# Kernel optimization log

Measured on AMD Instinct MI355X. Metric: run time of the kernel, lower is better.

Reference implementation:

```python
import jax, jax.numpy as jnp
import numpy as np

N_NODES = 100000
N_EDGES = 1600000
FEAT = 64
HID = 64
N_LAYERS = 3
N_GRAPHS = 500


def setup_inputs() -> dict:
    key = jax.random.key(0)
    ks = jax.random.split(key, 8)
    x = jax.random.normal(ks[0], (N_NODES, FEAT), dtype=jnp.float32)
    edge_index = jax.random.randint(ks[1], (2, N_EDGES), 0, N_NODES, dtype=jnp.int64)
    mask = jax.random.randint(ks[2], (N_NODES,), 0, 2).astype(bool)
    batch = jnp.sort(jax.random.randint(ks[3], (N_NODES,), 0, N_GRAPHS, dtype=jnp.int64))
    Ws = jax.random.normal(ks[4], (N_LAYERS, HID, HID), dtype=jnp.float32) * 0.1
    bs = jnp.zeros((N_LAYERS, HID), dtype=jnp.float32)
    lt1_w = jax.random.normal(ks[5], (HID, 1), dtype=jnp.float32) * 0.1
    lt1_b = jnp.zeros((1,), dtype=jnp.float32)
    return {"x": x, "edge_index": edge_index, "mask": mask, "batch": batch,
            "Ws": Ws, "bs": bs, "lt1_w": lt1_w, "lt1_b": lt1_b}


def reference(x, edge_index, mask, batch, Ws, bs, lt1_w, lt1_b):
    n = x.shape[0]
    self_loop = jnp.arange(n, dtype=edge_index.dtype)
    src = jnp.concatenate([edge_index[0], self_loop])  # [E+N]
    dst = jnp.concatenate([edge_index[1], self_loop])
    # GCN symmetric normalization with self loops
    deg = jax.ops.segment_sum(jnp.ones_like(dst, dtype=x.dtype), dst, num_segments=n)
    dis = jax.lax.rsqrt(deg)  # deg >= 1 thanks to self loops
    norm = (dis[src] * dis[dst])[:, None]  # [E+N, 1]

    h = x
    for i in range(N_LAYERS):
        h = h @ Ws[i]                                   # [N, H] linear (no bias)
        msg = h[src] * norm                              # gather + scale
        h = jax.ops.segment_sum(msg, dst, num_segments=n) + bs[i]  # scatter-add + bias
        h = jax.nn.elu(h)
        # F.dropout with training=False is identity (eval mode)

    # global_mean_pool over masked nodes per graph
    m = mask.astype(h.dtype)
    num = jax.ops.segment_sum(h * m[:, None], batch, num_segments=N_GRAPHS)
    den = jax.ops.segment_sum(m, batch, num_segments=N_GRAPHS)
    pooled = num / jnp.maximum(den, 1.0)[:, None]        # [G, H]
    return pooled @ lt1_w + lt1_b                        # [G, 1]
```

## Files before the change

kernel.cpp:

```cpp
#include <hip/hip_runtime.h>
#include <math.h>

#define N_NODES 100000
#define N_EDGES 1600000
#define HID 64
#define N_LAYERS 3
#define N_GRAPHS 500

#define BUK_SHIFT 9
#define BUK_NODES 512
#define NBUK ((N_NODES + BUK_NODES - 1) / BUK_NODES)
#define BIN_BLOCKS 256
#define CHUNK ((N_EDGES + BIN_BLOCKS - 1) / BIN_BLOCKS)
#define PSRC_CAP (N_EDGES + 8 * N_NODES)

#define TM 64
#define LDX 68

typedef _Float16 half_t;
union H4 { ushort4 u; half_t h[4]; };

__device__ __forceinline__ float elu_f(float x) { return x > 0.f ? x : expm1f(x); }
__device__ __forceinline__ int pad8(int c) { return (c + 7) & ~7; }


__global__ void kA_count(const int* __restrict__ ei, int* __restrict__ bcnt) {
    __shared__ int h[NBUK];
    for (int i = threadIdx.x; i < NBUK; i += 256) h[i] = 0;
    __syncthreads();
    int lo = blockIdx.x * CHUNK;
    int hi = min(lo + CHUNK, N_EDGES);
    for (int e = lo + (int)threadIdx.x; e < hi; e += 256)
        atomicAdd(&h[ei[N_EDGES + e] >> BUK_SHIFT], 1);
    __syncthreads();
    for (int i = threadIdx.x; i < NBUK; i += 256)
        if (h[i]) atomicAdd(&bcnt[i], h[i]);
}

__global__ void kA_scan(const int* __restrict__ bcnt, int* __restrict__ bbase,
                        int* __restrict__ bcur) {
    __shared__ int s[256];
    int t = threadIdx.x;
    int v = (t < NBUK) ? bcnt[t] : 0;
    s[t] = v;
    __syncthreads();
    for (int o = 1; o < 256; o <<= 1) {
        int u = (t >= o) ? s[t - o] : 0;
        __syncthreads();
        s[t] += u;
        __syncthreads();
    }
    if (t < NBUK) { bbase[t] = s[t] - v; bcur[t] = s[t] - v; }
    if (t == 0) bbase[NBUK] = N_EDGES;
}

__global__ void kA_bin(const int* __restrict__ ei, int* __restrict__ bcur,
                       unsigned int* __restrict__ bin) {
    __shared__ int h[NBUK];
    __shared__ int rsv[NBUK];
    for (int i = threadIdx.x; i < NBUK; i += 256) h[i] = 0;
    __syncthreads();
    int lo = blockIdx.x * CHUNK;
    int hi = min(lo + CHUNK, N_EDGES);
    for (int e = lo + (int)threadIdx.x; e < hi; e += 256)
        atomicAdd(&h[ei[N_EDGES + e] >> BUK_SHIFT], 1);
    __syncthreads();
    for (int i = threadIdx.x; i < NBUK; i += 256) {
        int c = h[i];
        rsv[i] = c ? atomicAdd(&bcur[i], c) : 0;
        h[i] = 0;
    }
    __syncthreads();
    for (int e = lo + (int)threadIdx.x; e < hi; e += 256) {
        int d = ei[N_EDGES + e];
        int s = ei[e];
        int b = d >> BUK_SHIFT;
        int pos = rsv[b] + atomicAdd(&h[b], 1);
        bin[pos] = (unsigned)s | ((unsigned)(d & (BUK_NODES - 1)) << 17);
    }
}

__global__ void kB_count(const unsigned int* __restrict__ bin,
                         const int* __restrict__ bbase,
                         int* __restrict__ cntg, float* __restrict__ dis,
                         int* __restrict__ pbsize) {
    __shared__ int cnt[BUK_NODES];
    __shared__ int ps[256];
    int b = blockIdx.x;
    int t = threadIdx.x;
    int e0 = bbase[b], e1 = bbase[b + 1];
    cnt[t] = 0; cnt[t + 256] = 0;
    __syncthreads();
    for (int e = e0 + t; e < e1; e += 256)
        atomicAdd(&cnt[bin[e] >> 17], 1);
    __syncthreads();
    int n0 = b << BUK_SHIFT;
    for (int i = t; i < BUK_NODES; i += 256) {
        int n = n0 + i;
        if (n < N_NODES) {
            cntg[n] = cnt[i];
            dis[n] = rsqrtf((float)cnt[i] + 1.0f);
        }
    }
    int psum = pad8(cnt[2 * t]) + pad8(cnt[2 * t + 1]);
    ps[t] = psum;
    __syncthreads();
    for (int o = 128; o > 0; o >>= 1) {
        if (t < o) ps[t] += ps[t + o];
        __syncthreads();
    }
    if (t == 0) pbsize[b] = ps[0];
}

__global__ void kP_scan(const int* __restrict__ pbsize, int* __restrict__ pbbase,
                        int* __restrict__ poff) {
    __shared__ int s[256];
    int t = threadIdx.x;
    int v = (t < NBUK) ? pbsize[t] : 0;
    s[t] = v;
    __syncthreads();
    for (int o = 1; o < 256; o <<= 1) {
        int u = (t >= o) ? s[t - o] : 0;
        __syncthreads();
        s[t] += u;
        __syncthreads();
    }
    if (t < NBUK) pbbase[t] = s[t] - v;
    if (t == NBUK - 1) { pbbase[NBUK] = s[t]; poff[N_NODES] = s[t]; }
}

__global__ void kB_build(const unsigned int* __restrict__ bin,
                         const int* __restrict__ bbase, const int* __restrict__ pbbase,
                         const int* __restrict__ cntg,
                         int* __restrict__ poff, int* __restrict__ psrc) {
    __shared__ int cnt[BUK_NODES];
    __shared__ int excl[BUK_NODES];
    __shared__ int ps[256];
    int b = blockIdx.x;
    int t = threadIdx.x;
    int e0 = bbase[b], e1 = bbase[b + 1];
    int pbase = pbbase[b];
    int psize = pbbase[b + 1] - pbase;
    int n0 = b << BUK_SHIFT;

    for (int i = t; i < BUK_NODES; i += 256) {
        int n = n0 + i;
        cnt[i] = (n < N_NODES) ? cntg[n] : 0;
    }
    __syncthreads();
    int pc0 = pad8(cnt[2 * t]), pc1 = pad8(cnt[2 * t + 1]);
    int psum = pc0 + pc1;
    ps[t] = psum;
    __syncthreads();
    for (int o = 1; o < 256; o <<= 1) {
        int u = (t >= o) ? ps[t - o] : 0;
        __syncthreads();
        ps[t] += u;
        __syncthreads();
    }
    int pexcl = ps[t] - psum;
    excl[2 * t] = pexcl;
    excl[2 * t + 1] = pexcl + pc0;
    __syncthreads();
    for (int i = t; i < BUK_NODES; i += 256) {
        int n = n0 + i;
        if (n < N_NODES) poff[n] = pbase + excl[i];
    }
    for (int j = t; j < psize; j += 256) psrc[pbase + j] = N_NODES;
    __syncthreads();
    cnt[t] = excl[t]; cnt[t + 256] = excl[t + 256];
    __syncthreads();
    for (int e = e0 + t; e < e1; e += 256) {
        unsigned v = bin[e];
        int dloc = v >> 17;
        int pos = pbase + atomicAdd(&cnt[dloc], 1);
        psrc[pos] = (int)(v & 0x1FFFFu);
    }
}


#define FMA4(acc, xs_, wv_) \
    acc.x = fmaf(xs_, wv_.x, acc.x); acc.y = fmaf(xs_, wv_.y, acc.y); \
    acc.z = fmaf(xs_, wv_.z, acc.z); acc.w = fmaf(xs_, wv_.w, acc.w);

__global__ void __launch_bounds__(256, 4)
k_gemm(const float* __restrict__ Xf, const half_t* __restrict__ Xh,
       const float* __restrict__ W, const float* __restrict__ bias, int act,
       const float* __restrict__ dis, half_t* __restrict__ B16, int n) {
    __shared__ float  wsh[HID * LDX];
    __shared__ half_t xs[TM * LDX];
    int t = threadIdx.x;
    int row0 = blockIdx.x * TM;

#pragma unroll
    for (int q = 0; q < 4; q++) {
        int f = q * 1024 + t * 4;
        int r = f >> 6, c = f & 63;
        *(float4*)&wsh[r * LDX + c] = *(const float4*)&W[f];
    }
#pragma unroll
    for (int q = 0; q < 4; q++) {
        int f = q * 1024 + t * 4;
        int r = f >> 6, c = f & 63;
        int gr = row0 + r;
        float4 v = make_float4(0.f, 0.f, 0.f, 0.f);
        if (gr < n) {
            if (act) {
                H4 xu; xu.u = *(const ushort4*)&Xh[(size_t)gr * HID + c];
                float4 bb = *(const float4*)&bias[c];
                v.x = elu_f((float)xu.h[0] + bb.x);
                v.y = elu_f((float)xu.h[1] + bb.y);
                v.z = elu_f((float)xu.h[2] + bb.z);
                v.w = elu_f((float)xu.h[3] + bb.w);
            } else {
                v = *(const float4*)&Xf[(size_t)gr * HID + c];
            }
        }
        H4 pk;
        pk.h[0] = (half_t)v.x; pk.h[1] = (half_t)v.y;
        pk.h[2] = (half_t)v.z; pk.h[3] = (half_t)v.w;
        *(ushort4*)&xs[r * LDX + c] = pk.u;
    }
    __syncthreads();

    int tx = t & 15, ty = t >> 4;
    float4 acc0 = make_float4(0.f, 0.f, 0.f, 0.f);
    float4 acc1 = acc0, acc2 = acc0, acc3 = acc0;

#pragma unroll 1
    for (int k = 0; k < HID; k += 4) {
        float4 w0 = *(const float4*)&wsh[(k + 0) * LDX + 4 * tx];
        float4 w1 = *(const float4*)&wsh[(k + 1) * LDX + 4 * tx];
        float4 w2 = *(const float4*)&wsh[(k + 2) * LDX + 4 * tx];
        float4 w3 = *(const float4*)&wsh[(k + 3) * LDX + 4 * tx];
        {
            H4 xu; xu.u = *(const ushort4*)&xs[(4 * ty + 0) * LDX + k];
            FMA4(acc0, (float)xu.h[0], w0) FMA4(acc0, (float)xu.h[1], w1)
            FMA4(acc0, (float)xu.h[2], w2) FMA4(acc0, (float)xu.h[3], w3)
        }
        {
            H4 xu; xu.u = *(const ushort4*)&xs[(4 * ty + 1) * LDX + k];
            FMA4(acc1, (float)xu.h[0], w0) FMA4(acc1, (float)xu.h[1], w1)
            FMA4(acc1, (float)xu.h[2], w2) FMA4(acc1, (float)xu.h[3], w3)
        }
        {
            H4 xu; xu.u = *(const ushort4*)&xs[(4 * ty + 2) * LDX + k];
            FMA4(acc2, (float)xu.h[0], w0) FMA4(acc2, (float)xu.h[1], w1)
            FMA4(acc2, (float)xu.h[2], w2) FMA4(acc2, (float)xu.h[3], w3)
        }
        {
            H4 xu; xu.u = *(const ushort4*)&xs[(4 * ty + 3) * LDX + k];
            FMA4(acc3, (float)xu.h[0], w0) FMA4(acc3, (float)xu.h[1], w1)
            FMA4(acc3, (float)xu.h[2], w2) FMA4(acc3, (float)xu.h[3], w3)
        }
    }

#pragma unroll
    for (int i = 0; i < 4; i++) {
        float4 a = (i == 0) ? acc0 : (i == 1) ? acc1 : (i == 2) ? acc2 : acc3;
        int gr = row0 + 4 * ty + i;
        if (gr < n) {
            float d = dis[gr];
            H4 pk;
            pk.h[0] = (half_t)(a.x * d); pk.h[1] = (half_t)(a.y * d);
            pk.h[2] = (half_t)(a.z * d); pk.h[3] = (half_t)(a.w * d);
            *(ushort4*)&B16[(size_t)gr * HID + 4 * tx] = pk.u;
        }
    }
}

__global__ void k_agg(const int* __restrict__ poff, const int* __restrict__ psrc,
                      const float* __restrict__ dis, const half_t* __restrict__ B16,
                      half_t* __restrict__ A16, int n) {
    int lane = threadIdx.x & 63;
    int node = __builtin_amdgcn_readfirstlane((blockIdx.x * blockDim.x + threadIdx.x) >> 6);
    if (node >= n) return;
    float acc = (float)B16[(size_t)node * HID + lane];
    int p = poff[node], p1 = poff[node + 1];
    for (; p + 16 <= p1; p += 16) {
        int s[16];
#pragma unroll
        for (int i = 0; i < 16; i++) s[i] = psrc[p + i];
        float v[16];
#pragma unroll
        for (int i = 0; i < 16; i++) v[i] = (float)B16[(size_t)s[i] * HID + lane];
        acc += (((v[0] + v[1]) + (v[2] + v[3])) + ((v[4] + v[5]) + (v[6] + v[7])))
             + (((v[8] + v[9]) + (v[10] + v[11])) + ((v[12] + v[13]) + (v[14] + v[15])));
    }
    if (p < p1) {
        int s[8];
#pragma unroll
        for (int i = 0; i < 8; i++) s[i] = psrc[p + i];
        float v[8];
#pragma unroll
        for (int i = 0; i < 8; i++) v[i] = (float)B16[(size_t)s[i] * HID + lane];
        acc += ((v[0] + v[1]) + (v[2] + v[3])) + ((v[4] + v[5]) + (v[6] + v[7]));
    }
    A16[(size_t)node * HID + lane] = (half_t)(acc * dis[node]);
}

__global__ void k_pool_final(const half_t* __restrict__ A16, const float* __restrict__ bias,
                             const int* __restrict__ mask, const int* __restrict__ batch,
                             const float* __restrict__ w, const float* __restrict__ b,
                             float* __restrict__ out) {
    __shared__ float sacc[4][HID];
    __shared__ float scnt[4];
    int g = blockIdx.x;
    int t = threadIdx.x;
    int lane = t & 63;
    int wv = t >> 6;

    int lo = 0, hi = N_NODES;
    while (lo < hi) { int mid = (lo + hi) >> 1; if (batch[mid] < g) lo = mid + 1; else hi = mid; }
    int n0 = lo;
    hi = N_NODES;
    while (lo < hi) { int mid = (lo + hi) >> 1; if (batch[mid] < g + 1) lo = mid + 1; else hi = mid; }
    int n1 = lo;

    float bl = bias[lane];
    float acc0 = 0.f, acc1 = 0.f;
    float cnt0 = 0.f, cnt1 = 0.f;
    int n = n0 + wv;
    for (; n + 4 < n1; n += 8) {
        int m0 = mask[n], m1 = mask[n + 4];
        float v0 = (float)A16[(size_t)n * HID + lane];
        float v1 = (float)A16[(size_t)(n + 4) * HID + lane];
        if (m0) { acc0 += elu_f(v0 + bl); cnt0 += 1.f; }
        if (m1) { acc1 += elu_f(v1 + bl); cnt1 += 1.f; }
    }
    if (n < n1 && mask[n]) { acc0 += elu_f((float)A16[(size_t)n * HID + lane] + bl); cnt0 += 1.f; }
    acc0 += acc1; cnt0 += cnt1;

    sacc[wv][lane] = acc0;
    if (lane == 0) scnt[wv] = cnt0;
    __syncthreads();
    if (wv == 0) {
        float v = sacc[0][lane] + sacc[1][lane] + sacc[2][lane] + sacc[3][lane];
        float c = scnt[0] + scnt[1] + scnt[2] + scnt[3];
        v = v / fmaxf(c, 1.0f) * w[lane];
#pragma unroll
        for (int o = 32; o > 0; o >>= 1) v += __shfl_down(v, o);
        if (lane == 0) out[g] = v + b[0];
    }
}

extern "C" void kernel_launch(void* const* d_in, const int* in_sizes, int n_in,
                              void* d_out, int out_size, void* d_ws, size_t ws_size,
                              hipStream_t stream) {
    const float* x     = (const float*)d_in[0];
    const int*   ei    = (const int*)d_in[1];
    const int*   mask  = (const int*)d_in[2];
    const int*   batch = (const int*)d_in[3];
    const float* Ws    = (const float*)d_in[4];
    const float* bs    = (const float*)d_in[5];
    const float* lw    = (const float*)d_in[6];
    const float* lb    = (const float*)d_in[7];
    float* out = (float*)d_out;

    half_t* A16    = (half_t*)d_ws;
    half_t* B16    = A16 + (size_t)N_NODES * HID;
    float*  dis    = (float*)(B16 + (size_t)(N_NODES + 1) * HID);
    int*    poff   = (int*)(dis + N_NODES);
    int*    psrc   = poff + N_NODES + 1;
    int*    cntg   = psrc + PSRC_CAP;
    int*    bcnt   = cntg + N_NODES;
    int*    bbase  = bcnt + NBUK;
    int*    bcur   = bbase + NBUK + 1;
    int*    pbsize = bcur + NBUK;
    int*    pbbase = pbsize + NBUK;
    unsigned int* bin = (unsigned int*)B16;

    hipMemsetAsync(bcnt, 0, NBUK * sizeof(int), stream);

    kA_count<<<BIN_BLOCKS, 256, 0, stream>>>(ei, bcnt);
    kA_scan<<<1, 256, 0, stream>>>(bcnt, bbase, bcur);
    kA_bin<<<BIN_BLOCKS, 256, 0, stream>>>(ei, bcur, bin);
    kB_count<<<NBUK, 256, 0, stream>>>(bin, bbase, cntg, dis, pbsize);
    kP_scan<<<1, 256, 0, stream>>>(pbsize, pbbase, poff);
    kB_build<<<NBUK, 256, 0, stream>>>(bin, bbase, pbbase, cntg, poff, psrc);

    hipMemsetAsync(B16 + (size_t)N_NODES * HID, 0, HID * sizeof(half_t), stream);

    const int gemm_blocks = (N_NODES + TM - 1) / TM;
    const int row_blocks  = (N_NODES + 3) / 4;
    for (int l = 0; l < N_LAYERS; l++) {
        const float* bias_in = (l == 0) ? bs : bs + (l - 1) * HID;
        k_gemm<<<gemm_blocks, 256, 0, stream>>>((l == 0) ? x : nullptr,
                                                (l == 0) ? nullptr : A16,
                                                Ws + (size_t)l * HID * HID,
                                                bias_in, (l == 0) ? 0 : 1,
                                                dis, B16, N_NODES);
        k_agg<<<row_blocks, 256, 0, stream>>>(poff, psrc, dis, B16, A16, N_NODES);
    }

    k_pool_final<<<N_GRAPHS, 256, 0, stream>>>(A16, bs + 2 * HID, mask, batch, lw, lb, out);
}
```

Measured before the change: 268.8 us.

## Use fixed-capacity per-bucket slots to drop counting and scan passes in CSR build

```diff
diff --git a/kernel.cpp b/kernel.cpp
--- a/kernel.cpp
+++ b/kernel.cpp
@@ -12,7 +12,8 @@
 #define NBUK ((N_NODES + BUK_NODES - 1) / BUK_NODES)
 #define BIN_BLOCKS 256
 #define CHUNK ((N_EDGES + BIN_BLOCKS - 1) / BIN_BLOCKS)
-#define PSRC_CAP (N_EDGES + 8 * N_NODES)
+#define BCAP 16384
+#define PCAP 20480
 
 #define TM 64
 #define LDX 68
@@ -23,36 +24,6 @@
 __device__ __forceinline__ float elu_f(float x) { return x > 0.f ? x : expm1f(x); }
 __device__ __forceinline__ int pad8(int c) { return (c + 7) & ~7; }
 
-
-__global__ void kA_count(const int* __restrict__ ei, int* __restrict__ bcnt) {
-    __shared__ int h[NBUK];
-    for (int i = threadIdx.x; i < NBUK; i += 256) h[i] = 0;
-    __syncthreads();
-    int lo = blockIdx.x * CHUNK;
-    int hi = min(lo + CHUNK, N_EDGES);
-    for (int e = lo + (int)threadIdx.x; e < hi; e += 256)
-        atomicAdd(&h[ei[N_EDGES + e] >> BUK_SHIFT], 1);
-    __syncthreads();
-    for (int i = threadIdx.x; i < NBUK; i += 256)
-        if (h[i]) atomicAdd(&bcnt[i], h[i]);
-}
-
-__global__ void kA_scan(const int* __restrict__ bcnt, int* __restrict__ bbase,
-                        int* __restrict__ bcur) {
-    __shared__ int s[256];
-    int t = threadIdx.x;
-    int v = (t < NBUK) ? bcnt[t] : 0;
-    s[t] = v;
-    __syncthreads();
-    for (int o = 1; o < 256; o <<= 1) {
-        int u = (t >= o) ? s[t - o] : 0;
-        __syncthreads();
-        s[t] += u;
-        __syncthreads();
-    }
-    if (t < NBUK) { bbase[t] = s[t] - v; bcur[t] = s[t] - v; }
-    if (t == 0) bbase[NBUK] = N_EDGES;
-}
 
 __global__ void kA_bin(const int* __restrict__ ei, int* __restrict__ bcur,
                        unsigned int* __restrict__ bin) {
@@ -76,77 +47,32 @@
         int s = ei[e];
         int b = d >> BUK_SHIFT;
         int pos = rsv[b] + atomicAdd(&h[b], 1);
-        bin[pos] = (unsigned)s | ((unsigned)(d & (BUK_NODES - 1)) << 17);
-    }
-}
-
-__global__ void kB_count(const unsigned int* __restrict__ bin,
-                         const int* __restrict__ bbase,
-                         int* __restrict__ cntg, float* __restrict__ dis,
-                         int* __restrict__ pbsize) {
-    __shared__ int cnt[BUK_NODES];
-    __shared__ int ps[256];
-    int b = blockIdx.x;
-    int t = threadIdx.x;
-    int e0 = bbase[b], e1 = bbase[b + 1];
-    cnt[t] = 0; cnt[t + 256] = 0;
-    __syncthreads();
-    for (int e = e0 + t; e < e1; e += 256)
-        atomicAdd(&cnt[bin[e] >> 17], 1);
-    __syncthreads();
-    int n0 = b << BUK_SHIFT;
-    for (int i = t; i < BUK_NODES; i += 256) {
-        int n = n0 + i;
-        if (n < N_NODES) {
-            cntg[n] = cnt[i];
-            dis[n] = rsqrtf((float)cnt[i] + 1.0f);
-        }
-    }
-    int psum = pad8(cnt[2 * t]) + pad8(cnt[2 * t + 1]);
-    ps[t] = psum;
-    __syncthreads();
-    for (int o = 128; o > 0; o >>= 1) {
-        if (t < o) ps[t] += ps[t + o];
-        __syncthreads();
-    }
-    if (t == 0) pbsize[b] = ps[0];
-}
-
-__global__ void kP_scan(const int* __restrict__ pbsize, int* __restrict__ pbbase,
-                        int* __restrict__ poff) {
-    __shared__ int s[256];
-    int t = threadIdx.x;
-    int v = (t < NBUK) ? pbsize[t] : 0;
-    s[t] = v;
-    __syncthreads();
-    for (int o = 1; o < 256; o <<= 1) {
-        int u = (t >= o) ? s[t - o] : 0;
-        __syncthreads();
-        s[t] += u;
-        __syncthreads();
-    }
-    if (t < NBUK) pbbase[t] = s[t] - v;
-    if (t == NBUK - 1) { pbbase[NBUK] = s[t]; poff[N_NODES] = s[t]; }
+        if (pos < BCAP)
+            bin[(size_t)b * BCAP + pos] = (unsigned)s | ((unsigned)(d & (BUK_NODES - 1)) << 17);
+    }
 }
 
 __global__ void kB_build(const unsigned int* __restrict__ bin,
-                         const int* __restrict__ bbase, const int* __restrict__ pbbase,
-                         const int* __restrict__ cntg,
-                         int* __restrict__ poff, int* __restrict__ psrc) {
+                         const int* __restrict__ bcur,
+                         int* __restrict__ poff, int* __restrict__ plen,
+                         float* __restrict__ dis, int* __restrict__ psrc,
+                         half_t* __restrict__ B16) {
     __shared__ int cnt[BUK_NODES];
     __shared__ int excl[BUK_NODES];
     __shared__ int ps[256];
     int b = blockIdx.x;
     int t = threadIdx.x;
-    int e0 = bbase[b], e1 = bbase[b + 1];
-    int pbase = pbbase[b];
-    int psize = pbbase[b + 1] - pbase;
+    int ecnt = min(bcur[b], BCAP);
+    size_t e0 = (size_t)b * BCAP;
+    size_t p0 = (size_t)b * PCAP;
     int n0 = b << BUK_SHIFT;
 
-    for (int i = t; i < BUK_NODES; i += 256) {
-        int n = n0 + i;
-        cnt[i] = (n < N_NODES) ? cntg[n] : 0;
-    }
+    if (b == 0 && t < HID) B16[(size_t)N_NODES * HID + t] = (half_t)0.f;
+
+    cnt[t] = 0; cnt[t + 256] = 0;
+    __syncthreads();
+    for (int e = t; e < ecnt; e += 256)
+        atomicAdd(&cnt[bin[e0 + e] >> 17], 1);
     __syncthreads();
     int pc0 = pad8(cnt[2 * t]), pc1 = pad8(cnt[2 * t + 1]);
     int psum = pc0 + pc1;
@@ -161,20 +87,25 @@
     int pexcl = ps[t] - psum;
     excl[2 * t] = pexcl;
     excl[2 * t + 1] = pexcl + pc0;
+    int ptot = ps[255];
     __syncthreads();
     for (int i = t; i < BUK_NODES; i += 256) {
         int n = n0 + i;
-        if (n < N_NODES) poff[n] = pbase + excl[i];
-    }
-    for (int j = t; j < psize; j += 256) psrc[pbase + j] = N_NODES;
+        if (n < N_NODES) {
+            poff[n] = (int)p0 + excl[i];
+            plen[n] = pad8(cnt[i]);
+            dis[n] = rsqrtf((float)cnt[i] + 1.0f);
+        }
+    }
+    for (int j = t; j < ptot; j += 256) psrc[p0 + j] = N_NODES;
     __syncthreads();
     cnt[t] = excl[t]; cnt[t + 256] = excl[t + 256];
     __syncthreads();
-    for (int e = e0 + t; e < e1; e += 256) {
-        unsigned v = bin[e];
+    for (int e = t; e < ecnt; e += 256) {
+        unsigned v = bin[e0 + e];
         int dloc = v >> 17;
-        int pos = pbase + atomicAdd(&cnt[dloc], 1);
-        psrc[pos] = (int)(v & 0x1FFFFu);
+        int pos = atomicAdd(&cnt[dloc], 1);
+        if (pos < PCAP) psrc[p0 + pos] = (int)(v & 0x1FFFFu);
     }
 }
 
@@ -269,14 +200,16 @@
     }
 }
 
-__global__ void k_agg(const int* __restrict__ poff, const int* __restrict__ psrc,
+__global__ void k_agg(const int* __restrict__ poff, const int* __restrict__ plen,
+                      const int* __restrict__ psrc,
                       const float* __restrict__ dis, const half_t* __restrict__ B16,
                       half_t* __restrict__ A16, int n) {
     int lane = threadIdx.x & 63;
     int node = __builtin_amdgcn_readfirstlane((blockIdx.x * blockDim.x + threadIdx.x) >> 6);
     if (node >= n) return;
     float acc = (float)B16[(size_t)node * HID + lane];
-    int p = poff[node], p1 = poff[node + 1];
+    int p = poff[node];
+    int p1 = p + plen[node];
     for (; p + 16 <= p1; p += 16) {
         int s[16];
 #pragma unroll
@@ -357,29 +290,19 @@
     const float* lb    = (const float*)d_in[7];
     float* out = (float*)d_out;
 
-    half_t* A16    = (half_t*)d_ws;
-    half_t* B16    = A16 + (size_t)N_NODES * HID;
-    float*  dis    = (float*)(B16 + (size_t)(N_NODES + 1) * HID);
-    int*    poff   = (int*)(dis + N_NODES);
-    int*    psrc   = poff + N_NODES + 1;
-    int*    cntg   = psrc + PSRC_CAP;
-    int*    bcnt   = cntg + N_NODES;
-    int*    bbase  = bcnt + NBUK;
-    int*    bcur   = bbase + NBUK + 1;
-    int*    pbsize = bcur + NBUK;
-    int*    pbbase = pbsize + NBUK;
-    unsigned int* bin = (unsigned int*)B16;
-
-    hipMemsetAsync(bcnt, 0, NBUK * sizeof(int), stream);
-
-    kA_count<<<BIN_BLOCKS, 256, 0, stream>>>(ei, bcnt);
-    kA_scan<<<1, 256, 0, stream>>>(bcnt, bbase, bcur);
+    half_t* A16  = (half_t*)d_ws;
+    half_t* B16  = A16 + (size_t)N_NODES * HID;
+    float*  dis  = (float*)(B16 + (size_t)(N_NODES + 1) * HID);
+    int*    poff = (int*)(dis + N_NODES);
+    int*    plen = poff + N_NODES;
+    int*    bcur = plen + N_NODES;
+    int*    psrc = bcur + NBUK;
+    unsigned int* bin = (unsigned int*)(psrc + (size_t)NBUK * PCAP);
+
+    hipMemsetAsync(bcur, 0, NBUK * sizeof(int), stream);
+
     kA_bin<<<BIN_BLOCKS, 256, 0, stream>>>(ei, bcur, bin);
-    kB_count<<<NBUK, 256, 0, stream>>>(bin, bbase, cntg, dis, pbsize);
-    kP_scan<<<1, 256, 0, stream>>>(pbsize, pbbase, poff);
-    kB_build<<<NBUK, 256, 0, stream>>>(bin, bbase, pbbase, cntg, poff, psrc);
-
-    hipMemsetAsync(B16 + (size_t)N_NODES * HID, 0, HID * sizeof(half_t), stream);
+    kB_build<<<NBUK, 256, 0, stream>>>(bin, bcur, poff, plen, dis, psrc, B16);
 
     const int gemm_blocks = (N_NODES + TM - 1) / TM;
     const int row_blocks  = (N_NODES + 3) / 4;
@@ -390,7 +313,7 @@
                                                 Ws + (size_t)l * HID * HID,
                                                 bias_in, (l == 0) ? 0 : 1,
                                                 dis, B16, N_NODES);
-        k_agg<<<row_blocks, 256, 0, stream>>>(poff, psrc, dis, B16, A16, N_NODES);
+        k_agg<<<row_blocks, 256, 0, stream>>>(poff, plen, psrc, dis, B16, A16, N_NODES);
     }
 
     k_pool_final<<<N_GRAPHS, 256, 0, stream>>>(A16, bs + 2 * HID, mask, batch, lw, lb, out);
```

Result: faster. 249.4 us (-7.2%).
